# Kernel tuning notes

Measured on AMD Instinct MI355X. Metric: run time of the kernel, lower is better.

## Reference

```python
import jax, jax.numpy as jnp
import numpy as np

NEG_SLOPE = 0.2   # GATConv default leaky_relu slope
BN_EPS = 1e-5
N, D, H, DH, E, BS = 49152, 512, 8, 64, 131072, 12
N_LAYERS = 5  # conv6 exists in __init__ but is never called in forward


def setup_inputs() -> dict:
    key = jax.random.key(0)
    ks = jax.random.split(key, 12)
    s = 0.05
    x = jax.random.normal(ks[0], (N, D), jnp.float32)
    edge_index = jax.random.randint(ks[1], (2, E), 0, N, jnp.int64)
    Ws = jax.random.normal(ks[2], (N_LAYERS, D, H * DH), jnp.float32) * s
    Asrc = jax.random.normal(ks[3], (N_LAYERS, H, DH), jnp.float32) * s
    Adst = jax.random.normal(ks[4], (N_LAYERS, H, DH), jnp.float32) * s
    Bconv = jax.random.normal(ks[5], (N_LAYERS, H * DH), jnp.float32) * s
    Gamma = jnp.ones((N_LAYERS, D), jnp.float32)
    Beta = jnp.zeros((N_LAYERS, D), jnp.float32)
    Wl = jax.random.normal(ks[6], (D, 1), jnp.float32) * s
    bl = jnp.zeros((1,), jnp.float32)
    return {"x": x, "edge_index": edge_index, "Ws": Ws, "Asrc": Asrc,
            "Adst": Adst, "Bconv": Bconv, "Gamma": Gamma, "Beta": Beta,
            "Wl": Wl, "bl": bl, "bs": BS}


def _gat_conv(x, src, dst, W, a_src, a_dst, b):
    n = x.shape[0]
    h = (x @ W).reshape(n, H, DH)                      # [N,H,DH]
    al_s = jnp.einsum('nhd,hd->nh', h, a_src)          # [N,H]
    al_d = jnp.einsum('nhd,hd->nh', h, a_dst)
    e = jax.nn.leaky_relu(al_s[src] + al_d[dst], NEG_SLOPE)  # [Etot,H]
    # segment softmax over incoming edges of each dst node
    m = jax.ops.segment_max(e, dst, num_segments=n)
    p = jnp.exp(e - m[dst])
    z = jax.ops.segment_sum(p, dst, num_segments=n)
    alpha = p / (z[dst] + 1e-16)
    out = jax.ops.segment_sum(alpha[:, :, None] * h[src], dst, num_segments=n)
    return out.reshape(n, H * DH) + b


def _batch_norm(x, gamma, beta):
    mu = x.mean(0)
    var = x.var(0)  # biased, as torch BN uses for normalization
    return (x - mu) * jax.lax.rsqrt(var + BN_EPS) * gamma + beta


def reference(x, edge_index, Ws, Asrc, Adst, Bconv, Gamma, Beta, Wl, bl, bs):
    n = x.shape[0]
    loops = jnp.arange(n, dtype=edge_index.dtype)      # add_self_loops=True
    src = jnp.concatenate([edge_index[0], loops])
    dst = jnp.concatenate([edge_index[1], loops])
    for i in range(N_LAYERS):
        x = _gat_conv(x, src, dst, Ws[i], Asrc[i], Adst[i], Bconv[i])
        x = jax.nn.relu(_batch_norm(x, Gamma[i], Beta[i]))
    w = x @ Wl + bl                                    # [N,1]
    return w.reshape(bs, -1)
```

## Files before the change

### kernel.cpp

```cpp
#include <hip/hip_runtime.h>
#include <cstdint>

#define N_NODES 49152
#define DIM 512
#define NH 8
#define DHEAD 64
#define NE 131072
#define ETOT (NE + N_NODES)
#define NLAYERS 5
#define AGG_NODES 32
#define AGG_BLOCKS (N_NODES / AGG_NODES)

typedef short short8 __attribute__((ext_vector_type(8)));
typedef float floatx4 __attribute__((ext_vector_type(4)));

__device__ __forceinline__ float bf2f(unsigned short v) {
  union { unsigned int u; float f; } x; x.u = ((unsigned int)v) << 16; return x.f;
}
__device__ __forceinline__ unsigned short f2bf(float f) {
  union { float f; unsigned int u; } x; x.f = f;
  unsigned int r = x.u + 0x7fffu + ((x.u >> 16) & 1u);
  return (unsigned short)(r >> 16);
}
__device__ __forceinline__ void async_load16(const void* g, void* l) {
  __builtin_amdgcn_global_load_lds((const __attribute__((address_space(1))) void*)g,
                                   (__attribute__((address_space(3))) void*)l, 16, 0, 0);
}

__global__ __launch_bounds__(256) void convert_x_r8(const float* __restrict__ xf, unsigned short* __restrict__ xb)
{
  const size_t i = ((size_t)blockIdx.x * 256 + threadIdx.x) * 8;
  const float4 a = *(const float4*)&xf[i];
  const float4 b = *(const float4*)&xf[i + 4];
  unsigned int ov[4];
  ov[0] = (unsigned int)f2bf(a.x) | ((unsigned int)f2bf(a.y) << 16);
  ov[1] = (unsigned int)f2bf(a.z) | ((unsigned int)f2bf(a.w) << 16);
  ov[2] = (unsigned int)f2bf(b.x) | ((unsigned int)f2bf(b.y) << 16);
  ov[3] = (unsigned int)f2bf(b.z) | ((unsigned int)f2bf(b.w) << 16);
  *(uint4*)&xb[i] = *(const uint4*)ov;
}

__global__ void transpose_w_r8(const float* __restrict__ Ws, unsigned short* __restrict__ WT)
{
  __shared__ float tile[32][33];
  const int l  = blockIdx.z;
  const int nt = blockIdx.x * 32, kt = blockIdx.y * 32;
  const int tx = threadIdx.x & 31, ty = threadIdx.x >> 5;
  #pragma unroll
  for (int r = 0; r < 32; r += 8)
    tile[ty + r][tx] = Ws[(size_t)l*DIM*DIM + (size_t)(kt + ty + r)*DIM + nt + tx];
  __syncthreads();
  #pragma unroll
  for (int r = 0; r < 32; r += 8)
    WT[(size_t)l*DIM*DIM + (size_t)(nt + ty + r)*DIM + kt + tx] = f2bf(tile[tx][ty + r]);
}

__global__ void repack_edges_r8(const int* __restrict__ raw, int* __restrict__ eidx)
{
  const int i = blockIdx.x * 256 + threadIdx.x;
  bool is64 = true;
  #pragma unroll
  for (int j = 0; j < 16; j++) is64 = is64 && (raw[2*j + 1] == 0);
  int v;
  if (is64) v = (int)((const long long*)raw)[i];
  else      v = raw[i];
  eidx[i] = v;
}

__global__ void init_counts_r8(int* __restrict__ counts) {
  counts[blockIdx.x * 256 + threadIdx.x] = 1;
}
__global__ void hist_dst_r8(const int* __restrict__ eidx, int* __restrict__ counts) {
  const int i = blockIdx.x * 256 + threadIdx.x;
  atomicAdd(&counts[eidx[NE + i]], 1);
}
__global__ void scan_kernel_r8(const int* __restrict__ counts, int* __restrict__ offs, int* __restrict__ cursor)
{
  __shared__ int tot[1024];
  const int t = threadIdx.x;
  const int base = t * 48;
  int s = 0;
  for (int i = 0; i < 48; i++) s += counts[base + i];
  tot[t] = s;
  __syncthreads();
  for (int o = 1; o < 1024; o <<= 1) {
    int v = (t >= o) ? tot[t - o] : 0;
    __syncthreads();
    tot[t] += v;
    __syncthreads();
  }
  int run = tot[t] - s;
  for (int i = 0; i < 48; i++) {
    offs[base + i] = run;
    cursor[base + i] = run;
    run += counts[base + i];
  }
  if (t == 1023) offs[N_NODES] = tot[1023];
}
__global__ void scatter_edges_r8(const int* __restrict__ eidx, int* __restrict__ cursor, int* __restrict__ csrc)
{
  const int i = blockIdx.x * 256 + threadIdx.x;
  int s, d;
  if (i < NE) { s = eidx[i]; d = eidx[NE + i]; }
  else        { s = i - NE; d = s; }
  const int pos = atomicAdd(&cursor[d], 1);
  csrc[pos] = s;
}

__global__ __launch_bounds__(512, 4) void gemm_bt_r8(const unsigned short* __restrict__ A,
                                                     const unsigned short* __restrict__ BT,
                                                     const float* __restrict__ asrc,
                                                     const float* __restrict__ adst,
                                                     unsigned short* __restrict__ C,
                                                     float* __restrict__ als,
                                                     float* __restrict__ ald)
{
  __shared__ unsigned short As[128 * 64];
  __shared__ unsigned short Bs[256 * 64];
  const int m0 = blockIdx.x * 128;
  const int n0 = blockIdx.y * 256;
  const int tid = threadIdx.x;
  const int wv = tid >> 6, lane = tid & 63;
  const int wr = (wv & 1) * 64, wc = (wv >> 1) * 64;
  const int q = lane >> 4, c16 = lane & 15;
  const int arow = lane >> 3;
  const int acol = (lane & 7) * 8;

  floatx4 acc[4][4] = {};

  for (int k0 = 0; k0 < DIM; k0 += 64) {
    #pragma unroll
    for (int t = 0; t < 2; t++) {
      const int cb = wv * 2 + t;
      async_load16(A + (size_t)(m0 + cb*8 + arow)*DIM + k0 + acol, &As[cb * 512]);
    }
    #pragma unroll
    for (int t = 0; t < 4; t++) {
      const int cb = wv * 4 + t;
      async_load16(BT + (size_t)(n0 + cb*8 + arow)*DIM + k0 + acol, &Bs[cb * 512]);
    }
    __syncthreads();
    #pragma unroll
    for (int kk = 0; kk < 64; kk += 32) {
      short8 aF[4], bF[4];
      #pragma unroll
      for (int mt = 0; mt < 4; mt++)
        aF[mt] = *(const short8*)&As[(wr + mt*16 + c16) * 64 + kk + q*8];
      #pragma unroll
      for (int nt = 0; nt < 4; nt++)
        bF[nt] = *(const short8*)&Bs[(wc + nt*16 + c16) * 64 + kk + q*8];
      #pragma unroll
      for (int mt = 0; mt < 4; mt++)
        #pragma unroll
        for (int nt = 0; nt < 4; nt++)
          acc[mt][nt] = __builtin_amdgcn_mfma_f32_16x16x32_bf16(aF[mt], bF[nt], acc[mt][nt], 0, 0, 0);
    }
    __syncthreads();
  }
  #pragma unroll
  for (int mt = 0; mt < 4; mt++) {
    #pragma unroll
    for (int nt = 0; nt < 4; nt++) {
      const int col = n0 + wc + nt*16 + c16;
      #pragma unroll
      for (int r = 0; r < 4; r++) {
        const int row = m0 + wr + mt*16 + q*4 + r;
        C[(size_t)row * DIM + col] = f2bf(acc[mt][nt][r]);
      }
    }
  }
  const int head = 4 * blockIdx.y + (wc >> 6);
  float as_[4], ad_[4];
  #pragma unroll
  for (int nt = 0; nt < 4; nt++) {
    const int d = nt * 16 + c16;
    as_[nt] = asrc[head * DHEAD + d];
    ad_[nt] = adst[head * DHEAD + d];
  }
  #pragma unroll
  for (int mt = 0; mt < 4; mt++) {
    #pragma unroll
    for (int r = 0; r < 4; r++) {
      float ss = 0.f, sd = 0.f;
      #pragma unroll
      for (int nt = 0; nt < 4; nt++) {
        ss += acc[mt][nt][r] * as_[nt];
        sd += acc[mt][nt][r] * ad_[nt];
      }
      #pragma unroll
      for (int msk = 1; msk <= 8; msk <<= 1) {
        ss += __shfl_xor(ss, msk, 64);
        sd += __shfl_xor(sd, msk, 64);
      }
      if (c16 == 0) {
        const int row = m0 + wr + mt*16 + q*4 + r;
        als[row * NH + head] = ss;
        ald[row * NH + head] = sd;
      }
    }
  }
}

__global__ __launch_bounds__(256) void gat_agg_r8(const unsigned short* __restrict__ Hm,
    const float* __restrict__ als, const float* __restrict__ ald,
    const int* __restrict__ offs, const int* __restrict__ csrc,
    const float* __restrict__ bconv, unsigned short* __restrict__ Xout,
    float* __restrict__ ps, float* __restrict__ pq)
{
  __shared__ float red[4][1024];
  const int wv = threadIdx.x >> 6, lane = threadIdx.x & 63;
  const int hd = lane >> 3;
  const int hp = lane & 7;
  const int slot = lane >> 3;
  const float4 bA = ((const float4*)(bconv + (size_t)lane * 8))[0];
  const float4 bB = ((const float4*)(bconv + (size_t)lane * 8))[1];
  const float barr[8] = {bA.x, bA.y, bA.z, bA.w, bB.x, bB.y, bB.z, bB.w};
  float cs[8] = {}, cq[8] = {};

  for (int i = 0; i < 8; i++) {
    const int node = blockIdx.x * AGG_NODES + wv * 8 + i;
    const int e0 = offs[node], e1 = offs[node + 1];
    const int deg = e1 - e0;
    float acc[8] = {};
    float zinv;

    if (deg <= 64) {
      const float aldp = ald[node * NH + hp];
      const int myS = (lane < deg) ? csrc[e0 + lane] : 0;
      const int nr = (deg + 7) >> 3;
      float lgsto[8];
      #pragma unroll
      for (int r = 0; r < 8; r++) {
        if (r < nr) {
          const int k = r * 8 + slot;
          const int s = __shfl(myS, k & 63, 64);
          float lg = als[s * NH + hp] + aldp;
          lg = lg > 0.f ? lg : 0.2f * lg;
          lgsto[r] = (k < deg) ? lg : -1e30f;
        } else lgsto[r] = -1e30f;
      }
      float m = lgsto[0];
      #pragma unroll
      for (int r = 1; r < 8; r++) m = fmaxf(m, lgsto[r]);
      m = fmaxf(m, __shfl_xor(m, 8, 64));
      m = fmaxf(m, __shfl_xor(m, 16, 64));
      m = fmaxf(m, __shfl_xor(m, 32, 64));
      float z = 0.f;
      float wsto[8];
      #pragma unroll
      for (int r = 0; r < 8; r++) {
        if (r < nr) {
          const float w = __expf(lgsto[r] - m);
          wsto[r] = w; z += w;
        } else wsto[r] = 0.f;
      }
      z += __shfl_xor(z, 8, 64);
      z += __shfl_xor(z, 16, 64);
      z += __shfl_xor(z, 32, 64);
      const float zden = __shfl(z, hd, 64);
      zinv = 1.f / (zden + 1e-16f);

      int sn = __shfl(myS, 0, 64);
      uint4 hv = *(const uint4*)&Hm[(size_t)sn * DIM + lane * 8];
      #pragma unroll
      for (int r = 0; r < 8; r++) {
        if (r * 8 < deg) {
          const int kmax = (deg - r * 8 < 8) ? (deg - r * 8) : 8;
          for (int kk = 0; kk < kmax; kk++) {
            const uint4 hcur = hv;
            const int k = r * 8 + kk;
            if (k + 1 < deg) {
              const int s2 = __shfl(myS, (k + 1) & 63, 64);
              hv = *(const uint4*)&Hm[(size_t)s2 * DIM + lane * 8];
            }
            const float w = __shfl(wsto[r], (kk << 3) + hd, 64);
            const unsigned int* hpx = (const unsigned int*)&hcur;
            #pragma unroll
            for (int j = 0; j < 4; j++) {
              acc[2*j]   += w * bf2f((unsigned short)(hpx[j] & 0xffffu));
              acc[2*j+1] += w * bf2f((unsigned short)(hpx[j] >> 16));
            }
          }
        }
      }
    } else {
      const float aldv = ald[node * NH + hd];
      float m = -1e30f, z = 0.f;
      for (int e = e0; e < e1; e++) {
        const int s = csrc[e];
        float lg = als[s * NH + hd] + aldv;
        lg = lg > 0.f ? lg : 0.2f * lg;
        const float mn = fmaxf(m, lg);
        const float sf = __expf(m - mn);
        const float w  = __expf(lg - mn);
        z = z * sf + w;
        const uint4 hv = *(const uint4*)&Hm[(size_t)s * DIM + lane * 8];
        const unsigned int* hpx = (const unsigned int*)&hv;
        #pragma unroll
        for (int j = 0; j < 4; j++) {
          acc[2*j]   = acc[2*j]   * sf + w * bf2f((unsigned short)(hpx[j] & 0xffffu));
          acc[2*j+1] = acc[2*j+1] * sf + w * bf2f((unsigned short)(hpx[j] >> 16));
        }
        m = mn;
      }
      zinv = 1.f / (z + 1e-16f);
    }

    unsigned int ov[4];
    #pragma unroll
    for (int j = 0; j < 4; j++) {
      const unsigned short b0 = f2bf(acc[2*j] * zinv + barr[2*j]);
      const unsigned short b1 = f2bf(acc[2*j+1] * zinv + barr[2*j+1]);
      ov[j] = (unsigned int)b0 | ((unsigned int)b1 << 16);
      const float y0 = bf2f(b0), y1 = bf2f(b1);
      cs[2*j]   += y0; cq[2*j]   += y0 * y0;
      cs[2*j+1] += y1; cq[2*j+1] += y1 * y1;
    }
    *(uint4*)&Xout[(size_t)node * DIM + lane * 8] = *(const uint4*)ov;
  }
  #pragma unroll
  for (int j = 0; j < 8; j++) {
    red[wv][lane * 8 + j] = cs[j];
    red[wv][512 + lane * 8 + j] = cq[j];
  }
  __syncthreads();
  const int t = threadIdx.x;
  #pragma unroll
  for (int r = 0; r < 2; r++) {
    const int c = t + r * 256;
    ps[(size_t)blockIdx.x * 512 + c] = red[0][c] + red[1][c] + red[2][c] + red[3][c];
    pq[(size_t)blockIdx.x * 512 + c] = red[0][512+c] + red[1][512+c] + red[2][512+c] + red[3][512+c];
  }
}

__global__ __launch_bounds__(256) void bn_reduce_r8(const float* __restrict__ ps, const float* __restrict__ pq,
                                                    const float* __restrict__ gamma, const float* __restrict__ beta,
                                                    float* __restrict__ scale, float* __restrict__ shift)
{
  __shared__ float rs[256], rq[256];
  const int c = blockIdx.x;
  const int t = threadIdx.x;
  float s = 0.f, q = 0.f;
  for (int b = t; b < AGG_BLOCKS; b += 256) {
    s += ps[(size_t)b * 512 + c];
    q += pq[(size_t)b * 512 + c];
  }
  rs[t] = s; rq[t] = q;
  __syncthreads();
  for (int o = 128; o > 0; o >>= 1) {
    if (t < o) { rs[t] += rs[t + o]; rq[t] += rq[t + o]; }
    __syncthreads();
  }
  if (t == 0) {
    const float inv = 1.0f / (float)N_NODES;
    const float mean = rs[0] * inv;
    float var = rq[0] * inv - mean * mean;
    var = fmaxf(var, 0.f);
    const float rsq = rsqrtf(var + 1e-5f);
    const float sc = gamma[c] * rsq;
    scale[c] = sc;
    shift[c] = beta[c] - mean * sc;
  }
}

__global__ __launch_bounds__(256) void bn_apply_r8(unsigned short* __restrict__ X,
    const float* __restrict__ scale, const float* __restrict__ shift)
{
  const size_t i = ((size_t)blockIdx.x * 256 + threadIdx.x) * 8;
  const int c = (int)(i & (DIM - 1));
  uint4 v = *(const uint4*)&X[i];
  unsigned int* vp = (unsigned int*)&v;
  unsigned int ov[4];
  #pragma unroll
  for (int j = 0; j < 4; j++) {
    const float a = bf2f((unsigned short)(vp[j] & 0xffffu));
    const float b = bf2f((unsigned short)(vp[j] >> 16));
    const float ya = fmaxf(0.f, a * scale[c + 2*j]     + shift[c + 2*j]);
    const float yb = fmaxf(0.f, b * scale[c + 2*j + 1] + shift[c + 2*j + 1]);
    ov[j] = (unsigned int)f2bf(ya) | ((unsigned int)f2bf(yb) << 16);
  }
  *(uint4*)&X[i] = *(const uint4*)ov;
}

__global__ __launch_bounds__(256) void final_head_r8(const unsigned short* __restrict__ X,
    const float* __restrict__ scale, const float* __restrict__ shift,
    const float* __restrict__ wl, const float* __restrict__ blp,
    float* __restrict__ out)
{
  const int wv = threadIdx.x >> 6, lane = threadIdx.x & 63;
  const int node = blockIdx.x * 4 + wv;
  const uint4 xv = *(const uint4*)&X[(size_t)node * DIM + lane * 8];
  const unsigned int* xp = (const unsigned int*)&xv;
  const int c0 = lane * 8;
  float s = 0.f;
  #pragma unroll
  for (int i = 0; i < 4; i++) {
    const float a0 = bf2f((unsigned short)(xp[i] & 0xffffu));
    const float a1 = bf2f((unsigned short)(xp[i] >> 16));
    const float y0 = fmaxf(0.f, a0 * scale[c0 + 2*i]     + shift[c0 + 2*i]);
    const float y1 = fmaxf(0.f, a1 * scale[c0 + 2*i + 1] + shift[c0 + 2*i + 1]);
    s += y0 * wl[c0 + 2*i] + y1 * wl[c0 + 2*i + 1];
  }
  #pragma unroll
  for (int msk = 32; msk >= 1; msk >>= 1) s += __shfl_xor(s, msk, 64);
  if (lane == 0) out[node] = s + blp[0];
}

extern "C" void kernel_launch(void* const* d_in, const int* in_sizes, int n_in,
                              void* d_out, int out_size, void* d_ws, size_t ws_size,
                              hipStream_t stream)
{
  const float* x_in  = (const float*)d_in[0];
  const int*   ei    = (const int*)d_in[1];
  const float* Ws    = (const float*)d_in[2];
  const float* Asrc  = (const float*)d_in[3];
  const float* Adst  = (const float*)d_in[4];
  const float* Bconv = (const float*)d_in[5];
  const float* Gamma = (const float*)d_in[6];
  const float* Beta  = (const float*)d_in[7];
  const float* Wl    = (const float*)d_in[8];
  const float* bl    = (const float*)d_in[9];
  float* out = (float*)d_out;

  char* ws = (char*)d_ws;
  size_t off = 0;
  auto alloc = [&](size_t b) { char* p = ws + off; off += (b + 255) & ~(size_t)255; return p; };
  unsigned short* xbuf = (unsigned short*)alloc((size_t)N_NODES * DIM * 2);
  unsigned short* hbuf = (unsigned short*)alloc((size_t)N_NODES * DIM * 2);
  unsigned short* WT   = (unsigned short*)alloc((size_t)NLAYERS * DIM * DIM * 2);
  float* als   = (float*)alloc((size_t)N_NODES * NH * 4);
  float* ald   = (float*)alloc((size_t)N_NODES * NH * 4);
  int* eidx    = (int*)alloc((size_t)2 * NE * 4);
  int* counts  = (int*)alloc((size_t)N_NODES * 4);
  int* offs    = (int*)alloc(((size_t)N_NODES + 1) * 4);
  int* cursor  = (int*)alloc((size_t)N_NODES * 4);
  int* csrc    = (int*)alloc((size_t)ETOT * 4);
  float* ps    = (float*)alloc((size_t)AGG_BLOCKS * 512 * 4);
  float* pq    = (float*)alloc((size_t)AGG_BLOCKS * 512 * 4);
  float* scale = (float*)alloc(512 * 4);
  float* shift = (float*)alloc(512 * 4);

  convert_x_r8<<<(N_NODES * DIM / 8) / 256, 256, 0, stream>>>(x_in, xbuf);
  transpose_w_r8<<<dim3(16, 16, 5), 256, 0, stream>>>(Ws, WT);
  repack_edges_r8<<<(2 * NE) / 256, 256, 0, stream>>>(ei, eidx);
  init_counts_r8<<<N_NODES / 256, 256, 0, stream>>>(counts);
  hist_dst_r8<<<NE / 256, 256, 0, stream>>>(eidx, counts);
  scan_kernel_r8<<<1, 1024, 0, stream>>>(counts, offs, cursor);
  scatter_edges_r8<<<ETOT / 256, 256, 0, stream>>>(eidx, cursor, csrc);

  for (int l = 0; l < NLAYERS; l++) {
    gemm_bt_r8<<<dim3(N_NODES / 128, DIM / 256), 512, 0, stream>>>(
        xbuf, WT + (size_t)l * DIM * DIM,
        Asrc + l * NH * DHEAD, Adst + l * NH * DHEAD, hbuf, als, ald);
    gat_agg_r8<<<AGG_BLOCKS, 256, 0, stream>>>(hbuf, als, ald, offs, csrc,
                                               Bconv + l * DIM, xbuf, ps, pq);
    bn_reduce_r8<<<512, 256, 0, stream>>>(ps, pq, Gamma + l * DIM, Beta + l * DIM, scale, shift);
    if (l < NLAYERS - 1)
      bn_apply_r8<<<(N_NODES * DIM / 8) / 256, 256, 0, stream>>>(xbuf, scale, shift);
  }
  final_head_r8<<<N_NODES / 4, 256, 0, stream>>>(xbuf, scale, shift, Wl, bl, out);
}
```

Before: 881.3 us.

## Add low-degree fast path and use 8 waves per block in GAT aggregation

The aggregation kernel now runs 8 waves of 4 nodes each per block instead of 4 waves of 8 nodes, which raises latency hiding per block and changes the block-level BN partial reduction to sum 8 wave slices. It also adds a fast path for nodes with degree at most 8 (the common case, about 3.7 average with self loops). That path computes the softmax in a single round of shuffles and gathers four neighbour rows at once, so the loads are issued in parallel. The trade-off is more shared memory per block (32 KB), higher register pressure under launch bounds of 512, and a larger kernel with branch divergence between paths.

```diff
diff --git a/kernel.cpp b/kernel.cpp
--- a/kernel.cpp
+++ b/kernel.cpp
@@ -27,7 +27,7 @@
                                    (__attribute__((address_space(3))) void*)l, 16, 0, 0);
 }
 
-__global__ __launch_bounds__(256) void convert_x_r8(const float* __restrict__ xf, unsigned short* __restrict__ xb)
+__global__ __launch_bounds__(256) void convert_x_r9(const float* __restrict__ xf, unsigned short* __restrict__ xb)
 {
   const size_t i = ((size_t)blockIdx.x * 256 + threadIdx.x) * 8;
   const float4 a = *(const float4*)&xf[i];
@@ -40,7 +40,7 @@
   *(uint4*)&xb[i] = *(const uint4*)ov;
 }
 
-__global__ void transpose_w_r8(const float* __restrict__ Ws, unsigned short* __restrict__ WT)
+__global__ void transpose_w_r9(const float* __restrict__ Ws, unsigned short* __restrict__ WT)
 {
   __shared__ float tile[32][33];
   const int l  = blockIdx.z;
@@ -55,7 +55,7 @@
     WT[(size_t)l*DIM*DIM + (size_t)(nt + ty + r)*DIM + kt + tx] = f2bf(tile[tx][ty + r]);
 }
 
-__global__ void repack_edges_r8(const int* __restrict__ raw, int* __restrict__ eidx)
+__global__ void repack_edges_r9(const int* __restrict__ raw, int* __restrict__ eidx)
 {
   const int i = blockIdx.x * 256 + threadIdx.x;
   bool is64 = true;
@@ -67,14 +67,14 @@
   eidx[i] = v;
 }
 
-__global__ void init_counts_r8(int* __restrict__ counts) {
+__global__ void init_counts_r9(int* __restrict__ counts) {
   counts[blockIdx.x * 256 + threadIdx.x] = 1;
 }
-__global__ void hist_dst_r8(const int* __restrict__ eidx, int* __restrict__ counts) {
+__global__ void hist_dst_r9(const int* __restrict__ eidx, int* __restrict__ counts) {
   const int i = blockIdx.x * 256 + threadIdx.x;
   atomicAdd(&counts[eidx[NE + i]], 1);
 }
-__global__ void scan_kernel_r8(const int* __restrict__ counts, int* __restrict__ offs, int* __restrict__ cursor)
+__global__ void scan_kernel_r9(const int* __restrict__ counts, int* __restrict__ offs, int* __restrict__ cursor)
 {
   __shared__ int tot[1024];
   const int t = threadIdx.x;
@@ -97,7 +97,7 @@
   }
   if (t == 1023) offs[N_NODES] = tot[1023];
 }
-__global__ void scatter_edges_r8(const int* __restrict__ eidx, int* __restrict__ cursor, int* __restrict__ csrc)
+__global__ void scatter_edges_r9(const int* __restrict__ eidx, int* __restrict__ cursor, int* __restrict__ csrc)
 {
   const int i = blockIdx.x * 256 + threadIdx.x;
   int s, d;
@@ -107,7 +107,7 @@
   csrc[pos] = s;
 }
 
-__global__ __launch_bounds__(512, 4) void gemm_bt_r8(const unsigned short* __restrict__ A,
+__global__ __launch_bounds__(512, 4) void gemm_bt_r9(const unsigned short* __restrict__ A,
                                                      const unsigned short* __restrict__ BT,
                                                      const float* __restrict__ asrc,
                                                      const float* __restrict__ adst,
@@ -201,13 +201,13 @@
   }
 }
 
-__global__ __launch_bounds__(256) void gat_agg_r8(const unsigned short* __restrict__ Hm,
+__global__ __launch_bounds__(512, 4) void gat_agg_r9(const unsigned short* __restrict__ Hm,
     const float* __restrict__ als, const float* __restrict__ ald,
     const int* __restrict__ offs, const int* __restrict__ csrc,
     const float* __restrict__ bconv, unsigned short* __restrict__ Xout,
     float* __restrict__ ps, float* __restrict__ pq)
 {
-  __shared__ float red[4][1024];
+  __shared__ float red[8][1024];
   const int wv = threadIdx.x >> 6, lane = threadIdx.x & 63;
   const int hd = lane >> 3;
   const int hp = lane & 7;
@@ -217,14 +217,67 @@
   const float barr[8] = {bA.x, bA.y, bA.z, bA.w, bB.x, bB.y, bB.z, bB.w};
   float cs[8] = {}, cq[8] = {};
 
-  for (int i = 0; i < 8; i++) {
-    const int node = blockIdx.x * AGG_NODES + wv * 8 + i;
+  #pragma unroll 1
+  for (int i = 0; i < 4; i++) {
+    const int node = blockIdx.x * AGG_NODES + wv * 4 + i;
     const int e0 = offs[node], e1 = offs[node + 1];
     const int deg = e1 - e0;
     float acc[8] = {};
     float zinv;
 
-    if (deg <= 64) {
+    if (deg <= 8) {
+      const float aldp = ald[node * NH + hp];
+      const int myS = csrc[e0 + ((lane < deg) ? lane : 0)];
+      const int s_slot = __shfl(myS, slot, 64);
+      float lg = als[s_slot * NH + hp] + aldp;
+      lg = lg > 0.f ? lg : 0.2f * lg;
+      const float lgv = (slot < deg) ? lg : -1e30f;
+      float mx = fmaxf(lgv, __shfl_xor(lgv, 8, 64));
+      mx = fmaxf(mx, __shfl_xor(mx, 16, 64));
+      mx = fmaxf(mx, __shfl_xor(mx, 32, 64));
+      const float w = __expf(lgv - mx);
+      float z = w + __shfl_xor(w, 8, 64);
+      z += __shfl_xor(z, 16, 64);
+      z += __shfl_xor(z, 32, 64);
+      zinv = 1.f / (__shfl(z, hd, 64) + 1e-16f);
+
+      #pragma unroll
+      for (int g = 0; g < 2; g++) {
+        const int b = g * 4;
+        if (b < deg) {
+          const int k1 = (b+1 < deg) ? b+1 : 0;
+          const int k2 = (b+2 < deg) ? b+2 : 0;
+          const int k3 = (b+3 < deg) ? b+3 : 0;
+          const int s0 = __shfl(myS, b,  64);
+          const int s1 = __shfl(myS, k1, 64);
+          const int s2 = __shfl(myS, k2, 64);
+          const int s3 = __shfl(myS, k3, 64);
+          const uint4 h0v = *(const uint4*)&Hm[(size_t)s0 * DIM + lane * 8];
+          const uint4 h1v = *(const uint4*)&Hm[(size_t)s1 * DIM + lane * 8];
+          const uint4 h2v = *(const uint4*)&Hm[(size_t)s2 * DIM + lane * 8];
+          const uint4 h3v = *(const uint4*)&Hm[(size_t)s3 * DIM + lane * 8];
+          const float w0 = __shfl(w, (b+0)*8 + hd, 64);
+          const float w1 = __shfl(w, (b+1)*8 + hd, 64);
+          const float w2 = __shfl(w, (b+2)*8 + hd, 64);
+          const float w3 = __shfl(w, (b+3)*8 + hd, 64);
+          const unsigned int* p0 = (const unsigned int*)&h0v;
+          const unsigned int* p1 = (const unsigned int*)&h1v;
+          const unsigned int* p2 = (const unsigned int*)&h2v;
+          const unsigned int* p3 = (const unsigned int*)&h3v;
+          #pragma unroll
+          for (int j = 0; j < 4; j++) {
+            acc[2*j]   += w0 * bf2f((unsigned short)(p0[j] & 0xffffu))
+                        + w1 * bf2f((unsigned short)(p1[j] & 0xffffu))
+                        + w2 * bf2f((unsigned short)(p2[j] & 0xffffu))
+                        + w3 * bf2f((unsigned short)(p3[j] & 0xffffu));
+            acc[2*j+1] += w0 * bf2f((unsigned short)(p0[j] >> 16))
+                        + w1 * bf2f((unsigned short)(p1[j] >> 16))
+                        + w2 * bf2f((unsigned short)(p2[j] >> 16))
+                        + w3 * bf2f((unsigned short)(p3[j] >> 16));
+          }
+        }
+      }
+    } else if (deg <= 64) {
       const float aldp = ald[node * NH + hp];
       const int myS = (lane < deg) ? csrc[e0 + lane] : 0;
       const int nr = (deg + 7) >> 3;
@@ -257,8 +310,7 @@
       z += __shfl_xor(z, 8, 64);
       z += __shfl_xor(z, 16, 64);
       z += __shfl_xor(z, 32, 64);
-      const float zden = __shfl(z, hd, 64);
-      zinv = 1.f / (zden + 1e-16f);
+      zinv = 1.f / (__shfl(z, hd, 64) + 1e-16f);
 
       int sn = __shfl(myS, 0, 64);
       uint4 hv = *(const uint4*)&Hm[(size_t)sn * DIM + lane * 8];
@@ -325,15 +377,17 @@
   }
   __syncthreads();
   const int t = threadIdx.x;
-  #pragma unroll
-  for (int r = 0; r < 2; r++) {
-    const int c = t + r * 256;
-    ps[(size_t)blockIdx.x * 512 + c] = red[0][c] + red[1][c] + red[2][c] + red[3][c];
-    pq[(size_t)blockIdx.x * 512 + c] = red[0][512+c] + red[1][512+c] + red[2][512+c] + red[3][512+c];
-  }
-}
-
-__global__ __launch_bounds__(256) void bn_reduce_r8(const float* __restrict__ ps, const float* __restrict__ pq,
+  float s = 0.f, q = 0.f;
+  #pragma unroll
+  for (int w = 0; w < 8; w++) {
+    s += red[w][t];
+    q += red[w][512 + t];
+  }
+  ps[(size_t)blockIdx.x * 512 + t] = s;
+  pq[(size_t)blockIdx.x * 512 + t] = q;
+}
+
+__global__ __launch_bounds__(256) void bn_reduce_r9(const float* __restrict__ ps, const float* __restrict__ pq,
                                                     const float* __restrict__ gamma, const float* __restrict__ beta,
                                                     float* __restrict__ scale, float* __restrict__ shift)
 {
@@ -363,7 +417,7 @@
   }
 }
 
-__global__ __launch_bounds__(256) void bn_apply_r8(unsigned short* __restrict__ X,
+__global__ __launch_bounds__(256) void bn_apply_r9(unsigned short* __restrict__ X,
     const float* __restrict__ scale, const float* __restrict__ shift)
 {
   const size_t i = ((size_t)blockIdx.x * 256 + threadIdx.x) * 8;
@@ -382,7 +436,7 @@
   *(uint4*)&X[i] = *(const uint4*)ov;
 }
 
-__global__ __launch_bounds__(256) void final_head_r8(const unsigned short* __restrict__ X,
+__global__ __launch_bounds__(256) void final_head_r9(const unsigned short* __restrict__ X,
     const float* __restrict__ scale, const float* __restrict__ shift,
     const float* __restrict__ wl, const float* __restrict__ blp,
     float* __restrict__ out)
@@ -440,23 +494,23 @@
   float* scale = (float*)alloc(512 * 4);
   float* shift = (float*)alloc(512 * 4);
 
-  convert_x_r8<<<(N_NODES * DIM / 8) / 256, 256, 0, stream>>>(x_in, xbuf);
-  transpose_w_r8<<<dim3(16, 16, 5), 256, 0, stream>>>(Ws, WT);
-  repack_edges_r8<<<(2 * NE) / 256, 256, 0, stream>>>(ei, eidx);
-  init_counts_r8<<<N_NODES / 256, 256, 0, stream>>>(counts);
-  hist_dst_r8<<<NE / 256, 256, 0, stream>>>(eidx, counts);
-  scan_kernel_r8<<<1, 1024, 0, stream>>>(counts, offs, cursor);
-  scatter_edges_r8<<<ETOT / 256, 256, 0, stream>>>(eidx, cursor, csrc);
+  convert_x_r9<<<(N_NODES * DIM / 8) / 256, 256, 0, stream>>>(x_in, xbuf);
+  transpose_w_r9<<<dim3(16, 16, 5), 256, 0, stream>>>(Ws, WT);
+  repack_edges_r9<<<(2 * NE) / 256, 256, 0, stream>>>(ei, eidx);
+  init_counts_r9<<<N_NODES / 256, 256, 0, stream>>>(counts);
+  hist_dst_r9<<<NE / 256, 256, 0, stream>>>(eidx, counts);
+  scan_kernel_r9<<<1, 1024, 0, stream>>>(counts, offs, cursor);
+  scatter_edges_r9<<<ETOT / 256, 256, 0, stream>>>(eidx, cursor, csrc);
 
   for (int l = 0; l < NLAYERS; l++) {
-    gemm_bt_r8<<<dim3(N_NODES / 128, DIM / 256), 512, 0, stream>>>(
+    gemm_bt_r9<<<dim3(N_NODES / 128, DIM / 256), 512, 0, stream>>>(
         xbuf, WT + (size_t)l * DIM * DIM,
         Asrc + l * NH * DHEAD, Adst + l * NH * DHEAD, hbuf, als, ald);
-    gat_agg_r8<<<AGG_BLOCKS, 256, 0, stream>>>(hbuf, als, ald, offs, csrc,
+    gat_agg_r9<<<AGG_BLOCKS, 512, 0, stream>>>(hbuf, als, ald, offs, csrc,
                                                Bconv + l * DIM, xbuf, ps, pq);
-    bn_reduce_r8<<<512, 256, 0, stream>>>(ps, pq, Gamma + l * DIM, Beta + l * DIM, scale, shift);
+    bn_reduce_r9<<<512, 256, 0, stream>>>(ps, pq, Gamma + l * DIM, Beta + l * DIM, scale, shift);
     if (l < NLAYERS - 1)
-      bn_apply_r8<<<(N_NODES * DIM / 8) / 256, 256, 0, stream>>>(xbuf, scale, shift);
-  }
-  final_head_r8<<<N_NODES / 4, 256, 0, stream>>>(xbuf, scale, shift, Wl, bl, out);
-}
+      bn_apply_r9<<<(N_NODES * DIM / 8) / 256, 256, 0, stream>>>(xbuf, scale, shift);
+  }
+  final_head_r9<<<N_NODES / 4, 256, 0, stream>>>(xbuf, scale, shift, Wl, bl, out);
+}
```

New measurement: 812.5 us. 1.08x faster.
